# Kernel tuning notes

Hardware: AMD Instinct MI355X
Metric: run time of the kernel (lower is better)

## Reference

```python
import jax, jax.numpy as jnp
import numpy as np

SEQ = 4096
INPUT_DIM = 64
D_MODEL = 1024
LAYERS = 2


def setup_inputs() -> dict:
    key = jax.random.key(0)
    ks = jax.random.split(key, 7)
    s = 1.0 / np.sqrt(D_MODEL)  # torch-style uniform-ish scale, keeps gates unsaturated
    return {
        "input_market_values": jax.random.normal(ks[0], (SEQ, INPUT_DIM), jnp.float32),
        "W1": jax.random.normal(ks[1], (D_MODEL, INPUT_DIM), jnp.float32) / np.sqrt(INPUT_DIM),
        "b1": jax.random.normal(ks[2], (D_MODEL,), jnp.float32) * s,
        "Wih": jax.random.normal(ks[3], (LAYERS, 4 * D_MODEL, D_MODEL), jnp.float32) * s,
        "Whh": jax.random.normal(ks[4], (LAYERS, 4 * D_MODEL, D_MODEL), jnp.float32) * s,
        "bih": jax.random.normal(ks[5], (LAYERS, 4 * D_MODEL), jnp.float32) * s,
        "bhh": jax.random.normal(ks[6], (LAYERS, 4 * D_MODEL), jnp.float32) * s,
    }


def _lstm_layer(x, Wih, Whh, bih, bhh):
    # x: (T, H_in). PyTorch LSTM gate order: i, f, g, o.
    H = Whh.shape[1]
    b = bih + bhh
    xg = x @ Wih.T + b  # precompute input contribution for all timesteps: (T, 4H)

    def step(carry, xgt):
        h, c = carry
        g = xgt + h @ Whh.T
        i, f, gg, o = jnp.split(g, 4, axis=-1)
        c = jax.nn.sigmoid(f) * c + jax.nn.sigmoid(i) * jnp.tanh(gg)
        h = jax.nn.sigmoid(o) * jnp.tanh(c)
        return (h, c), h

    init = (jnp.zeros((H,), x.dtype), jnp.zeros((H,), x.dtype))
    _, hs = jax.lax.scan(step, init, xg)
    return hs  # (T, H)


def reference(input_market_values, W1, b1, Wih, Whh, bih, bhh):
    # Per-step Linear + LeakyReLU (equivalent to applying it to the whole sequence)
    x = jax.nn.leaky_relu(input_market_values @ W1.T + b1)  # (T, D)
    for l in range(Wih.shape[0]):  # small fixed number of layers
        x = _lstm_layer(x, Wih[l], Whh[l], bih[l], bhh[l])
    # Original returns leaky_relu of the top-layer output at the final timestep, shape (1,1,D)
    return jax.nn.leaky_relu(x[-1]).reshape(1, 1, -1)
```

## Files before the change

### kernel.cpp

```cpp
#include <hip/hip_runtime.h>
#include <hip/hip_fp16.h>
#include <math.h>

#define T_SEQ 4096
#define DIN   64
#define DM    1024
#define G4    4096
#define LSTRIDE_W ((size_t)G4 * DM)
#define LSTRIDE_B ((size_t)G4)

#define SENT16 0xDEADu
#define SENT32 0xDEADDEADu

#define S_RING  28
#define S_RETRY 6
#define S_HIST  8

typedef unsigned long long u64;
typedef unsigned int u32;
typedef unsigned short u16;

#define PAUSE(n) do { __builtin_amdgcn_s_sleep(n); asm volatile("" ::: "memory"); } while (0)

__device__ __forceinline__ float sigmoidf_(float x) {
    return 1.0f / (1.0f + __expf(-x));
}
__device__ __forceinline__ float tanhf_(float x) {
    float ax = fabsf(x);
    float e  = __expf(-2.0f * ax);
    float t  = (1.0f - e) / (1.0f + e);
    return copysignf(t, x);
}
__device__ __forceinline__ float lrelu_(float x) {
    return x > 0.0f ? x : 0.01f * x;
}

__device__ __forceinline__ u32 pk2_(float x, float y) {
    typedef __fp16 hv2 __attribute__((ext_vector_type(2)));
    union { hv2 h; u32 u; } c;
    c.h = __builtin_amdgcn_cvt_pkrtz(x, y);
    return c.u;
}
#if __has_builtin(__builtin_amdgcn_fdot2)
__device__ __forceinline__ float d2a_(u32 a, u32 b, float acc) {
    typedef __fp16 hv2 __attribute__((ext_vector_type(2)));
    union { u32 u; hv2 h; } ua, ub;
    ua.u = a; ub.u = b;
    return __builtin_amdgcn_fdot2(ua.h, ub.h, acc, false);
}
#else
__device__ __forceinline__ float d2a_(u32 a, u32 b, float acc) {
    union { u32 u; __half2 h; } ua, ub;
    ua.u = a; ub.u = b;
    float2 fa = __half22float2(ua.h);
    float2 fb = __half22float2(ub.h);
    return acc + fa.x * fb.x + fa.y * fb.y;
}
#endif
__device__ __forceinline__ float dot8a_(uint4 q, uint4 h, float acc) {
    acc = d2a_(q.x, h.x, acc);
    acc = d2a_(q.y, h.y, acc);
    acc = d2a_(q.z, h.z, acc);
    acc = d2a_(q.w, h.w, acc);
    return acc;
}
__device__ __forceinline__ bool has_sent_(u64 v) {
    return (((u32)v & 0xFFFFu) == SENT16) | ((((u32)v >> 16)) == SENT16) |
           (((u32)(v >> 32) & 0xFFFFu) == SENT16) | (((u32)(v >> 48)) == SENT16);
}

__global__ __launch_bounds__(256) void k_input(const float* __restrict__ inp,
                                               const float* __restrict__ W1,
                                               const float* __restrict__ b1,
                                               float* __restrict__ x) {
    __shared__ float s_in[DIN];
    const int t   = blockIdx.x;
    const int tid = threadIdx.x;
    if (tid < DIN) s_in[tid] = inp[(size_t)t * DIN + tid];
    __syncthreads();
#pragma unroll
    for (int q = 0; q < 4; q++) {
        const int d = tid + q * 256;
        const float4* wr = (const float4*)(W1 + (size_t)d * DIN);
        float acc = 0.0f;
#pragma unroll
        for (int e = 0; e < 16; e++) {
            float4 w = wr[e];
            acc += w.x * s_in[e * 4 + 0] + w.y * s_in[e * 4 + 1] +
                   w.z * s_in[e * 4 + 2] + w.w * s_in[e * 4 + 3];
        }
        acc += b1[d];
        x[(size_t)t * DM + d] = lrelu_(acc);
    }
}

__global__ __launch_bounds__(256) void k_gemm(const float* __restrict__ A,
                                              const float* __restrict__ B,
                                              const float* __restrict__ bih,
                                              const float* __restrict__ bhh,
                                              float* __restrict__ C) {
    const int K = DM;
    __shared__ float As[16][132];
    __shared__ float Bs[16][132];
    const int tid = threadIdx.x;
    const int m0 = blockIdx.y * 128, n0 = blockIdx.x * 128;
    const int tx = tid & 15, ty = tid >> 4;
    const int lr = tid >> 1;
    const int lc = (tid & 1) * 8;

    float acc[8][8] = {};
    const float4* ag = (const float4*)(A + (size_t)(m0 + lr) * K + lc);
    const float4* bg = (const float4*)(B + (size_t)(n0 + lr) * K + lc);

    for (int k0 = 0; k0 < K; k0 += 16) {
        float4 a0 = ag[0], a1 = ag[1];
        float4 b0 = bg[0], b1v = bg[1];
        ag += 4; bg += 4;
        __syncthreads();
        As[lc + 0][lr] = a0.x; As[lc + 1][lr] = a0.y; As[lc + 2][lr] = a0.z; As[lc + 3][lr] = a0.w;
        As[lc + 4][lr] = a1.x; As[lc + 5][lr] = a1.y; As[lc + 6][lr] = a1.z; As[lc + 7][lr] = a1.w;
        Bs[lc + 0][lr] = b0.x; Bs[lc + 1][lr] = b0.y; Bs[lc + 2][lr] = b0.z; Bs[lc + 3][lr] = b0.w;
        Bs[lc + 4][lr] = b1v.x; Bs[lc + 5][lr] = b1v.y; Bs[lc + 6][lr] = b1v.z; Bs[lc + 7][lr] = b1v.w;
        __syncthreads();
#pragma unroll
        for (int k = 0; k < 16; k++) {
            float a[8], b[8];
            *(float4*)&a[0] = *(const float4*)&As[k][ty * 8 + 0];
            *(float4*)&a[4] = *(const float4*)&As[k][ty * 8 + 4];
            *(float4*)&b[0] = *(const float4*)&Bs[k][tx * 8 + 0];
            *(float4*)&b[4] = *(const float4*)&Bs[k][tx * 8 + 4];
#pragma unroll
            for (int i = 0; i < 8; i++)
#pragma unroll
                for (int j = 0; j < 8; j++)
                    acc[i][j] += a[i] * b[j];
        }
    }
    float bj[8];
#pragma unroll
    for (int j = 0; j < 8; j++) {
        int n = n0 + tx * 8 + j;
        bj[j] = bih[n] + bhh[n];
    }
#pragma unroll
    for (int i = 0; i < 8; i++) {
        float4 v0, v1;
        v0.x = acc[i][0] + bj[0]; v0.y = acc[i][1] + bj[1];
        v0.z = acc[i][2] + bj[2]; v0.w = acc[i][3] + bj[3];
        v1.x = acc[i][4] + bj[4]; v1.y = acc[i][5] + bj[5];
        v1.z = acc[i][6] + bj[6]; v1.w = acc[i][7] + bj[7];
        float* cp = C + (size_t)(m0 + ty * 8 + i) * G4 + n0 + tx * 8;
        *(float4*)(cp + 0) = v0;
        *(float4*)(cp + 4) = v1;
    }
}

__global__ __launch_bounds__(256) void k_clear(u32* __restrict__ p) {
    uint4 v; v.x = SENT32; v.y = SENT32; v.z = SENT32; v.w = SENT32;
    ((uint4*)p)[(size_t)blockIdx.x * 256 + threadIdx.x] = v;
}

__global__ __launch_bounds__(1024, 1) void k_scan(
        const float* __restrict__ xg,
        const float* __restrict__ Wih1,
        const float* __restrict__ Whh0,
        const float* __restrict__ Whh1,
        const float* __restrict__ bih1,
        const float* __restrict__ bhh1,
        u16* h0h,
        u16* h1h,
        float* __restrict__ out) {
    const int tid   = threadIdx.x;
    const int rowid = tid >> 3;
    const int c     = tid & 7;
    const bool isL0 = (blockIdx.x < 32);

    __shared__ uint4 h0st[2][128];
    __shared__ uint4 h1st[2][128];
    __shared__ __align__(16) float pre[128];

    if (isL0) {
        const int w = blockIdx.x;
        const int g = rowid & 3, s = rowid >> 2;
        const int rg = g * DM + 32 * w + s;
        uint4 wq[16];
#pragma unroll
        for (int j = 0; j < 16; j++) {
            const float4* p = (const float4*)(Whh0 + (size_t)rg * DM + 8 * c + 64 * j);
            float4 a = p[0], b = p[1];
            wq[j].x = pk2_(a.x, a.y); wq[j].y = pk2_(a.z, a.w);
            wq[j].z = pk2_(b.x, b.y); wq[j].w = pk2_(b.z, b.w);
        }
        const bool stg = (tid >= 64 && tid < 320);
        const int  slot = tid - 64;
        const bool ldr = (c == 0);
        const bool pub = (tid < 32);
        float c0 = 0.f, h0v = 0.f;

        for (int t = 0; t < T_SEQ; t++) {
            const int par = t & 1;
            float xgv = 0.f;
            if (ldr) xgv = xg[(size_t)t * G4 + rg];

            if (t == 0) {
                if (stg) ((u64*)&h0st[0][0])[slot] = 0ull;
            } else if (stg) {
                PAUSE(S_RING);
                const u64* hp = (const u64*)(h0h + (size_t)(t - 1) * DM) + slot;
                u64 v;
                for (;;) {
                    v = __hip_atomic_load(hp, __ATOMIC_RELAXED, __HIP_MEMORY_SCOPE_AGENT);
                    if (!has_sent_(v)) break;
                    PAUSE(S_RETRY);
                }
                ((u64*)&h0st[par][0])[slot] = v;
            }
            __syncthreads();

            const uint4* hb = &h0st[par][0];
            float acc = 0.f;
#pragma unroll
            for (int j = 0; j < 16; j++)
                acc = dot8a_(wq[j], hb[c + 8 * j], acc);
            acc += __shfl_xor(acc, 1, 64);
            acc += __shfl_xor(acc, 2, 64);
            acc += __shfl_xor(acc, 4, 64);
            if (ldr) pre[rowid] = acc + xgv;
            __syncthreads();

            if (pub) {
                float4 p4 = *(const float4*)&pre[4 * tid];
                float i_ = sigmoidf_(p4.x), f_ = sigmoidf_(p4.y);
                float g_ = tanhf_(p4.z),   o_ = sigmoidf_(p4.w);
                c0  = f_ * c0 + i_ * g_;
                h0v = o_ * tanhf_(c0);
                u32 q = pk2_(h0v, h0v);
                __hip_atomic_store(h0h + (size_t)t * DM + 32 * w + tid,
                                   (u16)(q & 0xFFFFu),
                                   __ATOMIC_RELAXED, __HIP_MEMORY_SCOPE_AGENT);
            }
        }
    } else {
        const int u = blockIdx.x - 32;
        const int g = rowid & 3;
        const int m = (rowid >> 2) & 1;
        const int s = rowid >> 3;
        const float* WB = m ? Whh1 : Wih1;
        const int rg = g * DM + 16 * u + s;
        uint4 wq[16];
#pragma unroll
        for (int j = 0; j < 16; j++) {
            const float4* p = (const float4*)(WB + (size_t)rg * DM + 8 * c + 64 * j);
            float4 a = p[0], b = p[1];
            wq[j].x = pk2_(a.x, a.y); wq[j].y = pk2_(a.z, a.w);
            wq[j].z = pk2_(b.x, b.y); wq[j].w = pk2_(b.z, b.w);
        }
        float bsum[4] = {0.f, 0.f, 0.f, 0.f};
        if (tid < 16) {
#pragma unroll
            for (int gg = 0; gg < 4; gg++)
                bsum[gg] = bih1[gg * DM + 16 * u + tid] + bhh1[gg * DM + 16 * u + tid];
        }
        const bool st0 = (tid >= 64 && tid < 320);
        const int  sl0 = tid - 64;
        const bool st1 = (tid >= 320 && tid < 576);
        const int  sl1 = tid - 320;
        const bool ldr = (c == 0);
        const bool pub = (tid < 16);
        float c1 = 0.f, h1v = 0.f;

        for (int t = 0; t < T_SEQ; t++) {
            const int par = t & 1;

            if (st0) {
                const u64* hp = (const u64*)(h0h + (size_t)t * DM) + sl0;
                u64 v = __hip_atomic_load(hp, __ATOMIC_RELAXED, __HIP_MEMORY_SCOPE_AGENT);
                while (has_sent_(v)) {
                    PAUSE(S_HIST);
                    v = __hip_atomic_load(hp, __ATOMIC_RELAXED, __HIP_MEMORY_SCOPE_AGENT);
                }
                ((u64*)&h0st[par][0])[sl0] = v;
            }
            if (t == 0) {
                if (st1) ((u64*)&h1st[0][0])[sl1] = 0ull;
            } else if (st1) {
                PAUSE(S_RING);
                const u64* hp = (const u64*)(h1h + (size_t)(t - 1) * DM) + sl1;
                u64 v;
                for (;;) {
                    v = __hip_atomic_load(hp, __ATOMIC_RELAXED, __HIP_MEMORY_SCOPE_AGENT);
                    if (!has_sent_(v)) break;
                    PAUSE(S_RETRY);
                }
                ((u64*)&h1st[par][0])[sl1] = v;
            }
            __syncthreads();

            const uint4* hb = m ? &h1st[par][0] : &h0st[par][0];
            float acc = 0.f;
#pragma unroll
            for (int j = 0; j < 16; j++)
                acc = dot8a_(wq[j], hb[c + 8 * j], acc);
            acc += __shfl_xor(acc, 1, 64);
            acc += __shfl_xor(acc, 2, 64);
            acc += __shfl_xor(acc, 4, 64);
            if (ldr) pre[rowid] = acc;
            __syncthreads();

            if (pub) {
                float4 pa = *(const float4*)&pre[8 * tid];
                float4 pb = *(const float4*)&pre[8 * tid + 4];
                float pi = pa.x + pb.x + bsum[0];
                float pf = pa.y + pb.y + bsum[1];
                float pg = pa.z + pb.z + bsum[2];
                float po = pa.w + pb.w + bsum[3];
                float i_ = sigmoidf_(pi), f_ = sigmoidf_(pf);
                float g_ = tanhf_(pg),    o_ = sigmoidf_(po);
                c1  = f_ * c1 + i_ * g_;
                h1v = o_ * tanhf_(c1);
                u32 q = pk2_(h1v, h1v);
                __hip_atomic_store(h1h + (size_t)t * DM + 16 * u + tid,
                                   (u16)(q & 0xFFFFu),
                                   __ATOMIC_RELAXED, __HIP_MEMORY_SCOPE_AGENT);
            }
        }
        if (pub) out[16 * u + tid] = lrelu_(h1v);
    }
}

extern "C" void kernel_launch(void* const* d_in, const int* in_sizes, int n_in,
                              void* d_out, int out_size, void* d_ws, size_t ws_size,
                              hipStream_t stream) {
    const float* inp = (const float*)d_in[0];
    const float* W1  = (const float*)d_in[1];
    const float* b1  = (const float*)d_in[2];
    const float* Wih = (const float*)d_in[3];
    const float* Whh = (const float*)d_in[4];
    const float* bih = (const float*)d_in[5];
    const float* bhh = (const float*)d_in[6];
    float* out = (float*)d_out;

    float* x   = (float*)d_ws;
    float* xg  = x + (size_t)T_SEQ * DM;
    u16*   h0h = (u16*)d_ws;
    u16*   h1h = (u16*)d_ws + (size_t)T_SEQ * DM;
    (void)in_sizes; (void)n_in; (void)out_size; (void)ws_size;

    k_input<<<dim3(T_SEQ), dim3(256), 0, stream>>>(inp, W1, b1, x);

    k_gemm<<<dim3(32, 32), dim3(256), 0, stream>>>(x, Wih, bih, bhh, xg);

    k_clear<<<dim3(4096), dim3(256), 0, stream>>>((u32*)d_ws);

    k_scan<<<dim3(96), dim3(1024), 0, stream>>>(
        xg, Wih + LSTRIDE_W, Whh, Whh + LSTRIDE_W,
        bih + LSTRIDE_B, bhh + LSTRIDE_B, h0h, h1h, out);
}
```

Before: 8.879 ms.

## Split layer-0 recurrence across 64 blocks and apply gate activations in parallel

Layer 0 of the persistent LSTM scan now runs on 64 blocks of 16 hidden units each instead of 32 blocks of 32, so each thread holds half as many weight registers and the per-step dot product is shorter. The launch grows to 128 blocks. In both layers the gate sigmoid/tanh is now computed by the reducing lane per gate row, not serially by the publishing thread. The layer-1 Wih/Whh partial sums are combined with a cross-lane shuffle instead of through shared memory. The aim is a shorter serial critical path per timestep, at the cost of more blocks polling the shared hidden-state ring.

```diff
diff --git a/kernel.cpp b/kernel.cpp
--- a/kernel.cpp
+++ b/kernel.cpp
@@ -171,22 +171,22 @@
         u16* h1h,
         float* __restrict__ out) {
     const int tid   = threadIdx.x;
-    const int rowid = tid >> 3;
-    const int c     = tid & 7;
-    const bool isL0 = (blockIdx.x < 32);
+    const bool isL0 = (blockIdx.x < 64);
 
     __shared__ uint4 h0st[2][128];
     __shared__ uint4 h1st[2][128];
-    __shared__ __align__(16) float pre[128];
+    __shared__ __align__(16) float pre[64];
 
     if (isL0) {
-        const int w = blockIdx.x;
+        const int u = blockIdx.x;
+        const int c = tid & 15;
+        const int rowid = tid >> 4;
         const int g = rowid & 3, s = rowid >> 2;
-        const int rg = g * DM + 32 * w + s;
-        uint4 wq[16];
-#pragma unroll
-        for (int j = 0; j < 16; j++) {
-            const float4* p = (const float4*)(Whh0 + (size_t)rg * DM + 8 * c + 64 * j);
+        const int rg = g * DM + 16 * u + s;
+        uint4 wq[8];
+#pragma unroll
+        for (int j = 0; j < 8; j++) {
+            const float4* p = (const float4*)(Whh0 + (size_t)rg * DM + 8 * c + 128 * j);
             float4 a = p[0], b = p[1];
             wq[j].x = pk2_(a.x, a.y); wq[j].y = pk2_(a.z, a.w);
             wq[j].z = pk2_(b.x, b.y); wq[j].w = pk2_(b.z, b.w);
@@ -194,7 +194,7 @@
         const bool stg = (tid >= 64 && tid < 320);
         const int  slot = tid - 64;
         const bool ldr = (c == 0);
-        const bool pub = (tid < 32);
+        const bool pub = (tid < 16);
         float c0 = 0.f, h0v = 0.f;
 
         for (int t = 0; t < T_SEQ; t++) {
@@ -220,28 +220,32 @@
             const uint4* hb = &h0st[par][0];
             float acc = 0.f;
 #pragma unroll
-            for (int j = 0; j < 16; j++)
-                acc = dot8a_(wq[j], hb[c + 8 * j], acc);
+            for (int j = 0; j < 8; j++)
+                acc = dot8a_(wq[j], hb[c + 16 * j], acc);
             acc += __shfl_xor(acc, 1, 64);
             acc += __shfl_xor(acc, 2, 64);
             acc += __shfl_xor(acc, 4, 64);
-            if (ldr) pre[rowid] = acc + xgv;
+            acc += __shfl_xor(acc, 8, 64);
+            if (ldr) {
+                float pa = acc + xgv;
+                pre[rowid] = (g == 2) ? tanhf_(pa) : sigmoidf_(pa);
+            }
             __syncthreads();
 
             if (pub) {
-                float4 p4 = *(const float4*)&pre[4 * tid];
-                float i_ = sigmoidf_(p4.x), f_ = sigmoidf_(p4.y);
-                float g_ = tanhf_(p4.z),   o_ = sigmoidf_(p4.w);
-                c0  = f_ * c0 + i_ * g_;
-                h0v = o_ * tanhf_(c0);
+                float4 a4 = *(const float4*)&pre[4 * tid];
+                c0  = a4.y * c0 + a4.x * a4.z;
+                h0v = a4.w * tanhf_(c0);
                 u32 q = pk2_(h0v, h0v);
-                __hip_atomic_store(h0h + (size_t)t * DM + 32 * w + tid,
+                __hip_atomic_store(h0h + (size_t)t * DM + 16 * u + tid,
                                    (u16)(q & 0xFFFFu),
                                    __ATOMIC_RELAXED, __HIP_MEMORY_SCOPE_AGENT);
             }
         }
     } else {
-        const int u = blockIdx.x - 32;
+        const int u = blockIdx.x - 64;
+        const int c = tid & 7;
+        const int rowid = tid >> 3;
         const int g = rowid & 3;
         const int m = (rowid >> 2) & 1;
         const int s = rowid >> 3;
@@ -255,17 +259,13 @@
             wq[j].x = pk2_(a.x, a.y); wq[j].y = pk2_(a.z, a.w);
             wq[j].z = pk2_(b.x, b.y); wq[j].w = pk2_(b.z, b.w);
         }
-        float bsum[4] = {0.f, 0.f, 0.f, 0.f};
-        if (tid < 16) {
-#pragma unroll
-            for (int gg = 0; gg < 4; gg++)
-                bsum[gg] = bih1[gg * DM + 16 * u + tid] + bhh1[gg * DM + 16 * u + tid];
-        }
+        float bsel = 0.f;
+        if (c == 0 && m == 0)
+            bsel = bih1[g * DM + 16 * u + s] + bhh1[g * DM + 16 * u + s];
         const bool st0 = (tid >= 64 && tid < 320);
         const int  sl0 = tid - 64;
         const bool st1 = (tid >= 320 && tid < 576);
         const int  sl1 = tid - 320;
-        const bool ldr = (c == 0);
         const bool pub = (tid < 16);
         float c1 = 0.f, h1v = 0.f;
 
@@ -304,20 +304,17 @@
             acc += __shfl_xor(acc, 1, 64);
             acc += __shfl_xor(acc, 2, 64);
             acc += __shfl_xor(acc, 4, 64);
-            if (ldr) pre[rowid] = acc;
+            acc += __shfl_xor(acc, 32, 64);
+            if (c == 0 && m == 0) {
+                float pa = acc + bsel;
+                pre[4 * s + g] = (g == 2) ? tanhf_(pa) : sigmoidf_(pa);
+            }
             __syncthreads();
 
             if (pub) {
-                float4 pa = *(const float4*)&pre[8 * tid];
-                float4 pb = *(const float4*)&pre[8 * tid + 4];
-                float pi = pa.x + pb.x + bsum[0];
-                float pf = pa.y + pb.y + bsum[1];
-                float pg = pa.z + pb.z + bsum[2];
-                float po = pa.w + pb.w + bsum[3];
-                float i_ = sigmoidf_(pi), f_ = sigmoidf_(pf);
-                float g_ = tanhf_(pg),    o_ = sigmoidf_(po);
-                c1  = f_ * c1 + i_ * g_;
-                h1v = o_ * tanhf_(c1);
+                float4 a4 = *(const float4*)&pre[4 * tid];
+                c1  = a4.y * c1 + a4.x * a4.z;
+                h1v = a4.w * tanhf_(c1);
                 u32 q = pk2_(h1v, h1v);
                 __hip_atomic_store(h1h + (size_t)t * DM + 16 * u + tid,
                                    (u16)(q & 0xFFFFu),
@@ -352,7 +349,7 @@
 
     k_clear<<<dim3(4096), dim3(256), 0, stream>>>((u32*)d_ws);
 
-    k_scan<<<dim3(96), dim3(1024), 0, stream>>>(
+    k_scan<<<dim3(128), dim3(1024), 0, stream>>>(
         xg, Wih + LSTRIDE_W, Whh, Whh + LSTRIDE_W,
         bih + LSTRIDE_B, bhh + LSTRIDE_B, h0h, h1h, out);
 }
```

Measured after the change: 10.15 ms. +14.3%, slower.
